# Optimization experiments

Measured on AMD Instinct MI355X. Metric: run time of the kernel, lower is better.

Reference implementation:

```python
import jax, jax.numpy as jnp
import numpy as np

W = 1024          # hpm.W (Fourier window size)
D = 2 * W         # real-ified dimension
BATCH = 2048
P = 8             # number of previous windows
OMEGA = 50        # sparsity level kept by hard threshold
N_ITERS = 10
L = 1.0           # hpm.L (Lipschitz constant, non-learnable)
CLAMP = 150.0


def setup_inputs() -> dict:
    key = jax.random.key(0)
    k1, k2, k3 = jax.random.split(key, 3)
    x = jax.random.normal(k1, (BATCH, D), jnp.float32)
    prev_windows = jax.random.normal(k2, (P, BATCH, D), jnp.float32)
    # learnable dictionary (Fourier-initialized in the original; random orthogonal-ish here)
    W_d = jax.random.normal(k3, (D, D), jnp.float32) / np.float32(np.sqrt(D))
    # S = I - (1/L) W_d^T W_d, exactly as in __init__
    S = jnp.eye(D, dtype=jnp.float32) - (1.0 / L) * (W_d.T @ W_d)
    lambda2 = jnp.array(1.0, jnp.float32)
    return {"x": x, "prev_windows": prev_windows, "W_d": W_d, "S": S, "lambda2": lambda2}


def _hard_thr(v):
    # keep the OMEGA largest-|.| entries along the last axis, zero the rest
    a = jnp.abs(v)
    kth = jax.lax.top_k(a, OMEGA)[0][..., -1:]  # (batch, 1) threshold
    return jnp.where(a >= kth, v, jnp.zeros_like(v))


def reference(x, prev_windows, W_d, S, lambda2):
    # B = (1/L) W_d x         (batch, D); z vectors kept as (batch, D), last dim == the
    # original dim=-2 since trailing singleton dim is squeezed away.
    B = (1.0 / L) * jnp.einsum('ij,bj->bi', W_d, x)
    z = _hard_thr(B)
    z = _hard_thr(B + jnp.einsum('ij,bj->bi', S, z))

    # attention over previous windows
    s_t = jnp.einsum('ji,bj->bi', W_d, z)                       # W_d^T z : (batch, D)
    s_prev = jnp.einsum('ij,pbj->pbi', W_d, prev_windows)       # (P, batch, D)
    # diagonal of (P,batch,batch) matmul == per-(p,b) dot product; compute it directly
    att = jnp.einsum('pbd,bd->pb', s_prev, s_t)                 # (P, batch)
    att = jax.nn.softmax(att, axis=1)
    pw = jnp.clip(prev_windows, -CLAMP, CLAMP)
    z = lambda2 * jnp.sum(pw * att[..., None], axis=0)          # (batch, D)

    # LIHT iterations; only zs[-1] is used downstream, so carry only the last z
    def step(zc, _):
        zn = _hard_thr(B + jnp.einsum('ij,bj->bi', S, zc))
        return zn, None
    z_last, _ = jax.lax.scan(step, z, None, length=N_ITERS)

    # complex power spectrum: sign flip on imag part does not change the norm
    cpx = z_last.reshape(BATCH, 2, W)
    p = cpx[:, 0, :] ** 2 + cpx[:, 1, :] ** 2                   # (batch, W)
    mD = p.sum(0)                                               # (W,)
    mD_norm = (mD - mD.min()) / (mD.max() - mD.min() + 1e-8)
    return mD_norm, z_last
```

## Files before the change

kernel.cpp:

```cpp
#include <hip/hip_runtime.h>


#define DD 2048
#define NB 2048
#define PLANE ((size_t)1 << 22)
#define ZONE 49152

using short8v  = __attribute__((ext_vector_type(8))) short;
using ushort8v = __attribute__((ext_vector_type(8))) unsigned short;
using ushort4v = __attribute__((ext_vector_type(4))) unsigned short;
using float4v  = __attribute__((ext_vector_type(4))) float;

__device__ __forceinline__ unsigned short f2bf(float f) {
  unsigned u = __float_as_uint(f);
  u = u + 0x7fffu + ((u >> 16) & 1u);
  return (unsigned short)(u >> 16);
}
__device__ __forceinline__ float bf2f(unsigned short h) {
  return __uint_as_float((unsigned)h << 16);
}
__device__ __forceinline__ void gload16(const void* g, void* l) {
  __builtin_amdgcn_global_load_lds((const __attribute__((address_space(1))) void*)g,
                                   (__attribute__((address_space(3))) void*)l,
                                   16, 0, 0);
}

template<int R>
__global__ __launch_bounds__(256)
void conv3T(const float* __restrict__ in, unsigned short* __restrict__ p0,
            unsigned short* __restrict__ p1, unsigned short* __restrict__ p2) {
  __shared__ unsigned short lds3[3][4][R][8];
  const int rt = blockIdx.x, c = blockIdx.y, t = threadIdx.x;
  const int cf = (t & 7) * 4;
  const int g = cf >> 3, e0 = cf & 7;
#pragma unroll
  for (int pass = 0; pass < R / 32; ++pass) {
    const int r = pass * 32 + (t >> 3);
    float4 v = *(const float4*)(in + (size_t)(rt * R + r) * DD + c * 32 + cf);
    float vv[4] = {v.x, v.y, v.z, v.w};
    ushort4v o0, o1, o2;
#pragma unroll
    for (int j = 0; j < 4; ++j) {
      unsigned short a0 = f2bf(vv[j]); float r1 = vv[j] - bf2f(a0);
      unsigned short a1 = f2bf(r1);    float r2 = r1 - bf2f(a1);
      unsigned short a2 = f2bf(r2);
      o0[j] = a0; o1[j] = a1; o2[j] = a2;
    }
    *(ushort4v*)&lds3[0][g][r][e0] = o0;
    *(ushort4v*)&lds3[1][g][r][e0] = o1;
    *(ushort4v*)&lds3[2][g][r][e0] = o2;
  }
  __syncthreads();
  const ushort8v* src = (const ushort8v*)lds3;
  const size_t tb = ((size_t)rt * 64 + c) * (R * 32);
#pragma unroll
  for (int w = 0; w < (3 * R) / 64; ++w) {
    const int idx = w * 256 + t;
    const int p = idx / (4 * R), off = idx % (4 * R);
    unsigned short* dst = (p == 0 ? p0 : p == 1 ? p1 : p2) + tb + (size_t)off * 8;
    *(ushort8v*)dst = src[idx];
  }
}

__global__ __launch_bounds__(256)
void tconv3(const float* __restrict__ in, unsigned short* __restrict__ p0,
            unsigned short* __restrict__ p1, unsigned short* __restrict__ p2) {
  __shared__ unsigned short lds3[3][4][64][8];
  const int nt = blockIdx.x, c = blockIdx.y, t = threadIdx.x;
  const int nf = (t & 15) * 4;
#pragma unroll
  for (int pass = 0; pass < 2; ++pass) {
    const int kr = pass * 16 + (t >> 4);
    float4 v = *(const float4*)(in + (size_t)(c * 32 + kr) * DD + nt * 64 + nf);
    float vv[4] = {v.x, v.y, v.z, v.w};
    const int g = kr >> 3, e = kr & 7;
#pragma unroll
    for (int j = 0; j < 4; ++j) {
      unsigned short a0 = f2bf(vv[j]); float r1 = vv[j] - bf2f(a0);
      unsigned short a1 = f2bf(r1);    float r2 = r1 - bf2f(a1);
      unsigned short a2 = f2bf(r2);
      lds3[0][g][nf + j][e] = a0;
      lds3[1][g][nf + j][e] = a1;
      lds3[2][g][nf + j][e] = a2;
    }
  }
  __syncthreads();
  const ushort8v* src = (const ushort8v*)lds3;
  const size_t tb = ((size_t)nt * 64 + c) * 2048;
#pragma unroll
  for (int w = 0; w < 3; ++w) {
    const int idx = w * 256 + t;
    const int p = idx >> 8, off = idx & 255;
    unsigned short* dst = (p == 0 ? p0 : p == 1 ? p1 : p2) + tb + (size_t)off * 8;
    *(ushort8v*)dst = src[idx];
  }
}

template<int ADD>
__global__ __launch_bounds__(512)
void gemm_bf6(const unsigned short* __restrict__ PA,
              const unsigned short* __restrict__ PB,
              const float* __restrict__ Cadd, float* __restrict__ Cout) {
  __shared__ char lds[3 * ZONE];
  const int tid = threadIdx.x, lane = tid & 63, wid = tid >> 6;

  const int lin = (int)blockIdx.x;
  const int xcd = lin & 7, q = lin >> 3;
  const int mt = (xcd >> 1) * 4 + (q >> 3);
  const int nt = (xcd & 1) * 8 + (q & 7);
  const int m0 = mt * 128, n0 = nt * 128;

  auto stage = [&](char* base, int c) {
    if (wid < 4) {
      const size_t at = ((size_t)mt * 64 + c) * 4096;
#pragma unroll
      for (int i = 0; i < 6; ++i) {
        const int slot = wid * 6 + i, p = slot >> 3, j = slot & 7;
        gload16(PA + p * PLANE + at + j * 512 + lane * 8,
                base + p * 8192 + j * 1024 + lane * 16);
      }
    } else {
#pragma unroll
      for (int i = 0; i < 6; ++i) {
        const int b = (wid - 4) * 6 + i, p = b >> 3, r = b & 7;
        const int sub = r >> 2, j = r & 3;
        const size_t bt = ((size_t)(nt * 2 + sub) * 64 + c) * 2048;
        gload16(PB + p * PLANE + bt + j * 512 + lane * 8,
                base + 24576 + p * 8192 + sub * 4096 + j * 1024 + lane * 16);
      }
    }
  };

  float4v acc[4][2] = {};

  const int rsel = (wid >> 2) * 64;
  const int csel = (wid & 3) * 32;
  const int g16  = lane >> 4;
  const int l15  = lane & 15;
  const int aoff = g16 * 2048 + (rsel + l15) * 16;
  const int boff = 24576 + (csel >> 6) * 4096 + g16 * 1024
                 + ((csel & 32) + l15) * 16;

  stage(lds, 0);
  stage(lds + ZONE, 1);

  int zc = 0, zs = 2;
  for (int c = 0; c < 64; ++c) {
    if (c + 2 < 64) stage(lds + zs * ZONE, c + 2);
    if (c + 2 < 64)      asm volatile("s_waitcnt vmcnt(12)" ::: "memory");
    else if (c + 1 < 64) asm volatile("s_waitcnt vmcnt(6)"  ::: "memory");
    else                 asm volatile("s_waitcnt vmcnt(0)"  ::: "memory");
    __builtin_amdgcn_s_barrier();
    __builtin_amdgcn_sched_barrier(0);

    const char* cur = lds + zc * ZONE;
    short8v b0[2], b1[2], b2[2];
#pragma unroll
    for (int ng = 0; ng < 2; ++ng) {
      b0[ng] = *(const short8v*)(cur + boff + 0 * 8192 + ng * 256);
      b1[ng] = *(const short8v*)(cur + boff + 1 * 8192 + ng * 256);
      b2[ng] = *(const short8v*)(cur + boff + 2 * 8192 + ng * 256);
    }
#pragma unroll
    for (int mg = 0; mg < 4; ++mg) {
      const short8v a0 = *(const short8v*)(cur + 0 * 8192 + aoff + mg * 256);
      const short8v a1 = *(const short8v*)(cur + 1 * 8192 + aoff + mg * 256);
      const short8v a2 = *(const short8v*)(cur + 2 * 8192 + aoff + mg * 256);
#pragma unroll
      for (int ng = 0; ng < 2; ++ng) {
        float4v t = acc[mg][ng];
        t = __builtin_amdgcn_mfma_f32_16x16x32_bf16(a0, b0[ng], t, 0, 0, 0);
        t = __builtin_amdgcn_mfma_f32_16x16x32_bf16(a0, b1[ng], t, 0, 0, 0);
        t = __builtin_amdgcn_mfma_f32_16x16x32_bf16(a1, b0[ng], t, 0, 0, 0);
        t = __builtin_amdgcn_mfma_f32_16x16x32_bf16(a1, b1[ng], t, 0, 0, 0);
        t = __builtin_amdgcn_mfma_f32_16x16x32_bf16(a0, b2[ng], t, 0, 0, 0);
        t = __builtin_amdgcn_mfma_f32_16x16x32_bf16(a2, b0[ng], t, 0, 0, 0);
        acc[mg][ng] = t;
      }
    }
    __builtin_amdgcn_sched_barrier(0);
    __builtin_amdgcn_s_barrier();
    zc = (zc == 2) ? 0 : zc + 1;
    zs = (zs == 2) ? 0 : zs + 1;
  }

  const int row0 = m0 + rsel + g16 * 4;
  const int col0 = n0 + csel + l15;
#pragma unroll
  for (int mg = 0; mg < 4; ++mg)
#pragma unroll
    for (int ng = 0; ng < 2; ++ng)
#pragma unroll
      for (int r = 0; r < 4; ++r) {
        const size_t o = (size_t)(row0 + mg * 16 + r) * DD + col0 + ng * 16;
        float v = acc[mg][ng][r];
        if (ADD) v += Cadd[o];
        Cout[o] = v;
      }
}

template<int HASBASE>
__global__ __launch_bounds__(64)
void spapply_sl(const float* __restrict__ M, const float* __restrict__ baseB,
                float* __restrict__ outF, const unsigned* __restrict__ sidx,
                const float* __restrict__ sval, const int* __restrict__ scnt) {
  const int b = blockIdx.y, lane = threadIdx.x;
  const int col = blockIdx.x * 256 + lane * 4;
  const int nc = scnt[b];
  const unsigned* ip = sidx + b * 64;
  const float* vp = sval + b * 64;
  const size_t ro = (size_t)b * DD + col;
  float4 a;
  if (HASBASE) a = *(const float4*)&baseB[ro];
  else         a = make_float4(0.f, 0.f, 0.f, 0.f);
  for (int t = 0; t < nc; ++t) {
    const unsigned j = ip[t];
    const float v = vp[t];
    float4 m = *(const float4*)&M[(size_t)j * DD + col];
    a.x = fmaf(v, m.x, a.x); a.y = fmaf(v, m.y, a.y);
    a.z = fmaf(v, m.z, a.z); a.w = fmaf(v, m.w, a.w);
  }
  *(float4*)&outF[ro] = a;
}

__global__ __launch_bounds__(64)
void topk_kernel(const float* __restrict__ src, unsigned* __restrict__ sidx,
                 float* __restrict__ sval, int* __restrict__ scnt,
                 float* __restrict__ dense, float* __restrict__ mD,
                 int finalMode) {
  const int b = blockIdx.x;
  const int lane = threadIdx.x;
  const float* row = src + (size_t)b * DD;
  float v[32]; unsigned ab[32];
#pragma unroll
  for (int e4 = 0; e4 < 8; ++e4) {
    float4 t = *(const float4*)&row[e4*256 + lane*4];
    v[e4*4+0]=t.x; v[e4*4+1]=t.y; v[e4*4+2]=t.z; v[e4*4+3]=t.w;
  }
#pragma unroll
  for (int e = 0; e < 32; ++e) ab[e] = __float_as_uint(v[e]) & 0x7fffffffu;

  unsigned mxb = 0;
#pragma unroll
  for (int e = 0; e < 32; ++e) mxb = ab[e] > mxb ? ab[e] : mxb;
  for (int off = 32; off; off >>= 1) {
    unsigned o = (unsigned)__shfl_down((int)mxb, off);
    mxb = o > mxb ? o : mxb;
  }
  mxb = (unsigned)__shfl((int)mxb, 0);
  const int emax = (int)(mxb >> 23);

  int eStar = 0, cntAbove = 0;
  {
    int prevc = 0;
    for (int e = emax; e >= 0; --e) {
      unsigned T = ((unsigned)e) << 23;
      int c = 0;
#pragma unroll
      for (int k = 0; k < 32; ++k) c += (ab[k] >= T) ? 1 : 0;
      for (int off = 32; off; off >>= 1) c += __shfl_down(c, off);
      c = __shfl(c, 0);
      if (c >= 50) { eStar = e; cntAbove = prevc; break; }
      prevc = c;
    }
  }
  unsigned kth = ((unsigned)eStar) << 23;
  int kneed = 50 - cntAbove;

  __shared__ int hist[256];
  __shared__ int sh_sel, sh_kneed;
  for (int p = 0; p < 3; ++p) {
    const unsigned mask = (p==0) ? 0x7F800000u : (p==1) ? 0x7FFF8000u : 0x7FFFFF80u;
    const int sh = (p==0) ? 15 : (p==1) ? 7 : 0;
    for (int t = lane; t < 256; t += 64) hist[t] = 0;
    __syncthreads();
#pragma unroll
    for (int e = 0; e < 32; ++e)
      if ((ab[e] & mask) == kth) atomicAdd(&hist[(ab[e] >> sh) & 0xFF], 1);
    __syncthreads();
    int h0 = hist[lane*4+0], h1 = hist[lane*4+1], h2 = hist[lane*4+2], h3 = hist[lane*4+3];
    int s = h0 + h1 + h2 + h3;
    int x = s;
    for (int off = 1; off < 64; off <<= 1) {
      int y = __shfl_down(x, off);
      if (lane + off < 64) x += y;
    }
    int excl = x - s;
    int c3 = excl + h3, c2 = c3 + h2, c1 = c2 + h1, c0 = c1 + h0;
    if (c0 >= kneed && c1   < kneed) { sh_sel = lane*4+0; sh_kneed = kneed - c1;  }
    if (c1 >= kneed && c2   < kneed) { sh_sel = lane*4+1; sh_kneed = kneed - c2;  }
    if (c2 >= kneed && c3   < kneed) { sh_sel = lane*4+2; sh_kneed = kneed - c3;  }
    if (c3 >= kneed && excl < kneed) { sh_sel = lane*4+3; sh_kneed = kneed - excl;}
    __syncthreads();
    kth |= ((unsigned)sh_sel) << sh;
    kneed = sh_kneed;
    __syncthreads();
  }

  int base = 0;
#pragma unroll
  for (int e4 = 0; e4 < 8; ++e4) {
    float o[4];
#pragma unroll
    for (int qq = 0; qq < 4; ++qq) {
      const int e = e4*4 + qq;
      const bool sel = ab[e] >= kth;
      unsigned long long msk = __ballot(sel);
      int pre = __popcll(msk & ((1ull << lane) - 1ull));
      const unsigned gi = (unsigned)(e4*256 + lane*4 + qq);
      if (sel) {
        int slot = base + pre;
        if (slot < 64) { sidx[b*64+slot] = gi; sval[b*64+slot] = v[e]; }
        if (finalMode) atomicAdd(&mD[gi & 1023u], v[e]*v[e]);
      }
      base += __popcll(msk);
      o[qq] = sel ? v[e] : 0.f;
    }
    if (finalMode) {
      float4 t = {o[0],o[1],o[2],o[3]};
      *(float4*)&dense[(size_t)b*DD + e4*256 + lane*4] = t;
    }
  }
  if (lane == 0) scnt[b] = base < 64 ? base : 64;
}

__global__ __launch_bounds__(256)
void attdot_kernel(const float* __restrict__ prev, const float* __restrict__ U,
                   float* __restrict__ att) {
  const int b = blockIdx.x, p = blockIdx.y, tid = threadIdx.x;
  const float* pr = prev + ((size_t)p*NB + b) * DD;
  const float* u  = U + (size_t)b * DD;
  float s = 0.f;
#pragma unroll
  for (int h = 0; h < 2; ++h) {
    int i = (tid + h*256) * 4;
    float4 a = *(const float4*)&pr[i];
    float4 c = *(const float4*)&u[i];
    s += a.x*c.x + a.y*c.y + a.z*c.z + a.w*c.w;
  }
  for (int off = 32; off; off >>= 1) s += __shfl_down(s, off);
  __shared__ float ps[4];
  if ((tid & 63) == 0) ps[tid >> 6] = s;
  __syncthreads();
  if (tid == 0) att[(size_t)p*NB + b] = ps[0]+ps[1]+ps[2]+ps[3];
}

__global__ __launch_bounds__(256)
void softmax_kernel(const float* __restrict__ att, float* __restrict__ attw) {
  const int p = blockIdx.x, tid = threadIdx.x;
  const float* a = att + (size_t)p*NB;
  float loc[8]; float mx = -3.4e38f;
#pragma unroll
  for (int h = 0; h < 8; ++h) { loc[h] = a[tid + h*256]; mx = fmaxf(mx, loc[h]); }
  for (int off = 32; off; off >>= 1) mx = fmaxf(mx, __shfl_down(mx, off));
  __shared__ float ps[4]; __shared__ float sh_m, sh_s;
  if ((tid & 63) == 0) ps[tid >> 6] = mx;
  __syncthreads();
  if (tid == 0) sh_m = fmaxf(fmaxf(ps[0],ps[1]), fmaxf(ps[2],ps[3]));
  __syncthreads();
  const float m = sh_m;
  float sum = 0.f;
#pragma unroll
  for (int h = 0; h < 8; ++h) sum += expf(loc[h] - m);
  for (int off = 32; off; off >>= 1) sum += __shfl_down(sum, off);
  __syncthreads();
  if ((tid & 63) == 0) ps[tid >> 6] = sum;
  __syncthreads();
  if (tid == 0) sh_s = ps[0]+ps[1]+ps[2]+ps[3];
  __syncthreads();
  const float inv = 1.0f / sh_s;
#pragma unroll
  for (int h = 0; h < 8; ++h) attw[(size_t)p*NB + tid + h*256] = expf(loc[h] - m) * inv;
}

__global__ __launch_bounds__(256)
void zatt_kernel(const float* __restrict__ prev, const float* __restrict__ attw,
                 const float* __restrict__ lam, float* __restrict__ Z) {
  const int b = blockIdx.x, tid = threadIdx.x;
  __shared__ float w[8];
  if (tid < 8) w[tid] = attw[(size_t)tid*NB + b];
  __syncthreads();
  const float l2 = lam[0];
#pragma unroll
  for (int h = 0; h < 2; ++h) {
    int i = (tid + h*256) * 4;
    float4 acc = {0.f,0.f,0.f,0.f};
#pragma unroll
    for (int p = 0; p < 8; ++p) {
      float4 pv = *(const float4*)&prev[((size_t)p*NB + b)*DD + i];
      float wp = w[p];
      acc.x += wp * fminf(fmaxf(pv.x, -150.f), 150.f);
      acc.y += wp * fminf(fmaxf(pv.y, -150.f), 150.f);
      acc.z += wp * fminf(fmaxf(pv.z, -150.f), 150.f);
      acc.w += wp * fminf(fmaxf(pv.w, -150.f), 150.f);
    }
    acc.x *= l2; acc.y *= l2; acc.z *= l2; acc.w *= l2;
    *(float4*)&Z[(size_t)b*DD + i] = acc;
  }
}

__global__ __launch_bounds__(256)
void norm_kernel(float* __restrict__ mD) {
  const int tid = threadIdx.x;
  float v[4]; float mn = 3.4e38f, mx = -3.4e38f;
#pragma unroll
  for (int h = 0; h < 4; ++h) {
    v[h] = mD[tid + h*256];
    mn = fminf(mn, v[h]); mx = fmaxf(mx, v[h]);
  }
  for (int off = 32; off; off >>= 1) {
    mn = fminf(mn, __shfl_down(mn, off));
    mx = fmaxf(mx, __shfl_down(mx, off));
  }
  __shared__ float pmn[4], pmx[4]; __shared__ float smn, smx;
  if ((tid & 63) == 0) { pmn[tid>>6] = mn; pmx[tid>>6] = mx; }
  __syncthreads();
  if (tid == 0) {
    smn = fminf(fminf(pmn[0],pmn[1]), fminf(pmn[2],pmn[3]));
    smx = fmaxf(fmaxf(pmx[0],pmx[1]), fmaxf(pmx[2],pmx[3]));
  }
  __syncthreads();
  const float d = smx - smn + 1e-8f;
#pragma unroll
  for (int h = 0; h < 4; ++h) mD[tid + h*256] = (v[h] - smn) / d;
}

extern "C" void kernel_launch(void* const* d_in, const int* in_sizes, int n_in,
                              void* d_out, int out_size, void* d_ws, size_t ws_size,
                              hipStream_t stream) {
  const float* x    = (const float*)d_in[0];
  const float* prev = (const float*)d_in[1];
  const float* Wd   = (const float*)d_in[2];
  const float* S    = (const float*)d_in[3];
  const float* lam  = (const float*)d_in[4];

  float* out   = (float*)d_out;
  float* mD    = out;
  float* zlast = out + 1024;

  float* B  = (float*)d_ws;
  float* C  = B  + (1u << 22);
  float* X1 = C  + (1u << 22);
  unsigned* sidx = (unsigned*)(X1 + (1u << 22));
  float*    sval = (float*)(sidx + 2048*64);
  int*      scnt = (int*)(sval + 2048*64);
  float*    att  = (float*)(scnt + 2048);
  float*    attw = att + 8*2048;
  unsigned short* PA = (unsigned short*)(attw + 8*2048);
  unsigned short* PB = PA + 3 * PLANE;
  float* U = zlast;

  const dim3 gSp(8, NB);
  const dim3 gA(16, 64);
  const dim3 gB(32, 64);

  conv3T<128><<<gA, 256, 0, stream>>>(x,  PA, PA + PLANE, PA + 2*PLANE);
  conv3T<64> <<<gB, 256, 0, stream>>>(Wd, PB, PB + PLANE, PB + 2*PLANE);
  gemm_bf6<0><<<256, 512, 0, stream>>>(PA, PB, nullptr, B);
  topk_kernel<<<NB, 64, 0, stream>>>(B, sidx, sval, scnt, nullptr, nullptr, 0);
  spapply_sl<1><<<gSp, 64, 0, stream>>>(S, B, C, sidx, sval, scnt);
  topk_kernel<<<NB, 64, 0, stream>>>(C, sidx, sval, scnt, nullptr, nullptr, 0);
  spapply_sl<0><<<gSp, 64, 0, stream>>>(Wd, nullptr, X1, sidx, sval, scnt);
  conv3T<128><<<gA, 256, 0, stream>>>(X1, PA, PA + PLANE, PA + 2*PLANE);
  tconv3<<<gB, 256, 0, stream>>>(Wd, PB, PB + PLANE, PB + 2*PLANE);
  gemm_bf6<0><<<256, 512, 0, stream>>>(PA, PB, nullptr, U);
  attdot_kernel<<<dim3(NB, 8), 256, 0, stream>>>(prev, U, att);
  softmax_kernel<<<8, 256, 0, stream>>>(att, attw);
  zatt_kernel<<<NB, 256, 0, stream>>>(prev, attw, lam, X1);
  conv3T<128><<<gA, 256, 0, stream>>>(X1, PA, PA + PLANE, PA + 2*PLANE);
  conv3T<64> <<<gB, 256, 0, stream>>>(S,  PB, PB + PLANE, PB + 2*PLANE);
  gemm_bf6<1><<<256, 512, 0, stream>>>(PA, PB, B, C);
  topk_kernel<<<NB, 64, 0, stream>>>(C, sidx, sval, scnt, nullptr, nullptr, 0);
  for (int it = 1; it < 10; ++it) {
    spapply_sl<1><<<gSp, 64, 0, stream>>>(S, B, C, sidx, sval, scnt);
    const int fin = (it == 9);
    if (fin) hipMemsetAsync(mD, 0, 1024 * sizeof(float), stream);
    topk_kernel<<<NB, 64, 0, stream>>>(C, sidx, sval, scnt,
                                       fin ? zlast : nullptr,
                                       fin ? mD : nullptr, fin);
  }
  norm_kernel<<<1, 256, 0, stream>>>(mD);
}
```

Baseline: 1.218 ms.

## Use 4-wave GEMM tiles with single barrier and pipeline sparse row gathers

The bf16x3 GEMM now runs 256 threads per block. Each wave computes a 64x64 sub-tile, up from 64x32, so every A fragment feeds twice as many MFMAs. The next-stage prefetch is issued after the barrier, which drops the second per-iteration barrier, and the vmcnt waits are adjusted to match. The sparse-apply kernel now packs four rows per 256-thread block, stages the indices and values in LDS, and software-pipelines eight gathered float4 loads to raise memory-level parallelism. The trade-off is higher register pressure from the 4x4 accumulators and fewer waves per CU for the GEMM, plus the risk that one barrier per iteration is not enough to guard the triple-buffer reuse.

```diff
diff --git a/kernel.cpp b/kernel.cpp
--- a/kernel.cpp
+++ b/kernel.cpp
@@ -97,7 +97,7 @@
 }
 
 template<int ADD>
-__global__ __launch_bounds__(512)
+__global__ __launch_bounds__(256)
 void gemm_bf6(const unsigned short* __restrict__ PA,
               const unsigned short* __restrict__ PB,
               const float* __restrict__ Cadd, float* __restrict__ Cout) {
@@ -111,18 +111,18 @@
   const int m0 = mt * 128, n0 = nt * 128;
 
   auto stage = [&](char* base, int c) {
-    if (wid < 4) {
+    if (wid < 2) {
       const size_t at = ((size_t)mt * 64 + c) * 4096;
 #pragma unroll
-      for (int i = 0; i < 6; ++i) {
-        const int slot = wid * 6 + i, p = slot >> 3, j = slot & 7;
+      for (int i = 0; i < 12; ++i) {
+        const int slot = wid * 12 + i, p = slot >> 3, j = slot & 7;
         gload16(PA + p * PLANE + at + j * 512 + lane * 8,
                 base + p * 8192 + j * 1024 + lane * 16);
       }
     } else {
 #pragma unroll
-      for (int i = 0; i < 6; ++i) {
-        const int b = (wid - 4) * 6 + i, p = b >> 3, r = b & 7;
+      for (int i = 0; i < 12; ++i) {
+        const int bq = (wid - 2) * 12 + i, p = bq >> 3, r = bq & 7;
         const int sub = r >> 2, j = r & 3;
         const size_t bt = ((size_t)(nt * 2 + sub) * 64 + c) * 2048;
         gload16(PB + p * PLANE + bt + j * 512 + lane * 8,
@@ -131,32 +131,31 @@
     }
   };
 
-  float4v acc[4][2] = {};
-
-  const int rsel = (wid >> 2) * 64;
-  const int csel = (wid & 3) * 32;
+  float4v acc[4][4] = {};
+
+  const int rsel = (wid >> 1) * 64;
+  const int csel = (wid & 1) * 64;
   const int g16  = lane >> 4;
   const int l15  = lane & 15;
   const int aoff = g16 * 2048 + (rsel + l15) * 16;
-  const int boff = 24576 + (csel >> 6) * 4096 + g16 * 1024
-                 + ((csel & 32) + l15) * 16;
+  const int boff = 24576 + (csel >> 6) * 4096 + g16 * 1024 + l15 * 16;
 
   stage(lds, 0);
   stage(lds + ZONE, 1);
 
   int zc = 0, zs = 2;
   for (int c = 0; c < 64; ++c) {
-    if (c + 2 < 64) stage(lds + zs * ZONE, c + 2);
-    if (c + 2 < 64)      asm volatile("s_waitcnt vmcnt(12)" ::: "memory");
-    else if (c + 1 < 64) asm volatile("s_waitcnt vmcnt(6)"  ::: "memory");
-    else                 asm volatile("s_waitcnt vmcnt(0)"  ::: "memory");
+    if (c < 63) asm volatile("s_waitcnt vmcnt(12)" ::: "memory");
+    else        asm volatile("s_waitcnt vmcnt(0)"  ::: "memory");
     __builtin_amdgcn_s_barrier();
     __builtin_amdgcn_sched_barrier(0);
 
+    if (c + 2 < 64) stage(lds + zs * ZONE, c + 2);
+
     const char* cur = lds + zc * ZONE;
-    short8v b0[2], b1[2], b2[2];
-#pragma unroll
-    for (int ng = 0; ng < 2; ++ng) {
+    short8v b0[4], b1[4], b2[4];
+#pragma unroll
+    for (int ng = 0; ng < 4; ++ng) {
       b0[ng] = *(const short8v*)(cur + boff + 0 * 8192 + ng * 256);
       b1[ng] = *(const short8v*)(cur + boff + 1 * 8192 + ng * 256);
       b2[ng] = *(const short8v*)(cur + boff + 2 * 8192 + ng * 256);
@@ -167,7 +166,7 @@
       const short8v a1 = *(const short8v*)(cur + 1 * 8192 + aoff + mg * 256);
       const short8v a2 = *(const short8v*)(cur + 2 * 8192 + aoff + mg * 256);
 #pragma unroll
-      for (int ng = 0; ng < 2; ++ng) {
+      for (int ng = 0; ng < 4; ++ng) {
         float4v t = acc[mg][ng];
         t = __builtin_amdgcn_mfma_f32_16x16x32_bf16(a0, b0[ng], t, 0, 0, 0);
         t = __builtin_amdgcn_mfma_f32_16x16x32_bf16(a0, b1[ng], t, 0, 0, 0);
@@ -178,8 +177,6 @@
         acc[mg][ng] = t;
       }
     }
-    __builtin_amdgcn_sched_barrier(0);
-    __builtin_amdgcn_s_barrier();
     zc = (zc == 2) ? 0 : zc + 1;
     zs = (zs == 2) ? 0 : zs + 1;
   }
@@ -189,7 +186,7 @@
 #pragma unroll
   for (int mg = 0; mg < 4; ++mg)
 #pragma unroll
-    for (int ng = 0; ng < 2; ++ng)
+    for (int ng = 0; ng < 4; ++ng)
 #pragma unroll
       for (int r = 0; r < 4; ++r) {
         const size_t o = (size_t)(row0 + mg * 16 + r) * DD + col0 + ng * 16;
@@ -200,25 +197,54 @@
 }
 
 template<int HASBASE>
-__global__ __launch_bounds__(64)
+__global__ __launch_bounds__(256)
 void spapply_sl(const float* __restrict__ M, const float* __restrict__ baseB,
                 float* __restrict__ outF, const unsigned* __restrict__ sidx,
                 const float* __restrict__ sval, const int* __restrict__ scnt) {
-  const int b = blockIdx.y, lane = threadIdx.x;
+  const int lane = threadIdx.x & 63, w = threadIdx.x >> 6;
+  const int b = blockIdx.y * 4 + w;
   const int col = blockIdx.x * 256 + lane * 4;
+  __shared__ unsigned sj[4][64];
+  __shared__ float    sv[4][64];
+  sj[w][lane] = sidx[b * 64 + lane];
+  sv[w][lane] = sval[b * 64 + lane];
   const int nc = scnt[b];
-  const unsigned* ip = sidx + b * 64;
-  const float* vp = sval + b * 64;
+  __syncthreads();
+
   const size_t ro = (size_t)b * DD + col;
   float4 a;
   if (HASBASE) a = *(const float4*)&baseB[ro];
   else         a = make_float4(0.f, 0.f, 0.f, 0.f);
-  for (int t = 0; t < nc; ++t) {
-    const unsigned j = ip[t];
-    const float v = vp[t];
-    float4 m = *(const float4*)&M[(size_t)j * DD + col];
+
+  const float* Mc = M + col;
+  auto ld = [&](int t) -> float4 {
+    return *(const float4*)(Mc + (size_t)sj[w][t] * DD);
+  };
+  auto fma4 = [&](int t, const float4& m) {
+    const float v = sv[w][t];
     a.x = fmaf(v, m.x, a.x); a.y = fmaf(v, m.y, a.y);
     a.z = fmaf(v, m.z, a.z); a.w = fmaf(v, m.w, a.w);
+  };
+
+  float4 m[8];
+  int t = 0;
+  if (nc >= 8) {
+#pragma unroll
+    for (int i = 0; i < 8; ++i) m[i] = ld(i);
+    for (; t + 16 <= nc; t += 8) {
+#pragma unroll
+      for (int i = 0; i < 8; ++i) {
+        fma4(t + i, m[i]);
+        m[i] = ld(t + 8 + i);
+      }
+    }
+#pragma unroll
+    for (int i = 0; i < 8; ++i) fma4(t + i, m[i]);
+    t += 8;
+  }
+  for (; t < nc; ++t) {
+    float4 mm = ld(t);
+    fma4(t, mm);
   }
   *(float4*)&outF[ro] = a;
 }
@@ -450,29 +476,29 @@
   unsigned short* PB = PA + 3 * PLANE;
   float* U = zlast;
 
-  const dim3 gSp(8, NB);
+  const dim3 gSp(8, NB / 4);
   const dim3 gA(16, 64);
   const dim3 gB(32, 64);
 
   conv3T<128><<<gA, 256, 0, stream>>>(x,  PA, PA + PLANE, PA + 2*PLANE);
   conv3T<64> <<<gB, 256, 0, stream>>>(Wd, PB, PB + PLANE, PB + 2*PLANE);
-  gemm_bf6<0><<<256, 512, 0, stream>>>(PA, PB, nullptr, B);
+  gemm_bf6<0><<<256, 256, 0, stream>>>(PA, PB, nullptr, B);
   topk_kernel<<<NB, 64, 0, stream>>>(B, sidx, sval, scnt, nullptr, nullptr, 0);
-  spapply_sl<1><<<gSp, 64, 0, stream>>>(S, B, C, sidx, sval, scnt);
+  spapply_sl<1><<<gSp, 256, 0, stream>>>(S, B, C, sidx, sval, scnt);
   topk_kernel<<<NB, 64, 0, stream>>>(C, sidx, sval, scnt, nullptr, nullptr, 0);
-  spapply_sl<0><<<gSp, 64, 0, stream>>>(Wd, nullptr, X1, sidx, sval, scnt);
+  spapply_sl<0><<<gSp, 256, 0, stream>>>(Wd, nullptr, X1, sidx, sval, scnt);
   conv3T<128><<<gA, 256, 0, stream>>>(X1, PA, PA + PLANE, PA + 2*PLANE);
   tconv3<<<gB, 256, 0, stream>>>(Wd, PB, PB + PLANE, PB + 2*PLANE);
-  gemm_bf6<0><<<256, 512, 0, stream>>>(PA, PB, nullptr, U);
+  gemm_bf6<0><<<256, 256, 0, stream>>>(PA, PB, nullptr, U);
   attdot_kernel<<<dim3(NB, 8), 256, 0, stream>>>(prev, U, att);
   softmax_kernel<<<8, 256, 0, stream>>>(att, attw);
   zatt_kernel<<<NB, 256, 0, stream>>>(prev, attw, lam, X1);
   conv3T<128><<<gA, 256, 0, stream>>>(X1, PA, PA + PLANE, PA + 2*PLANE);
   conv3T<64> <<<gB, 256, 0, stream>>>(S,  PB, PB + PLANE, PB + 2*PLANE);
-  gemm_bf6<1><<<256, 512, 0, stream>>>(PA, PB, B, C);
+  gemm_bf6<1><<<256, 256, 0, stream>>>(PA, PB, B, C);
   topk_kernel<<<NB, 64, 0, stream>>>(C, sidx, sval, scnt, nullptr, nullptr, 0);
   for (int it = 1; it < 10; ++it) {
-    spapply_sl<1><<<gSp, 64, 0, stream>>>(S, B, C, sidx, sval, scnt);
+    spapply_sl<1><<<gSp, 256, 0, stream>>>(S, B, C, sidx, sval, scnt);
     const int fin = (it == 9);
     if (fin) hipMemsetAsync(mD, 0, 1024 * sizeof(float), stream);
     topk_kernel<<<NB, 64, 0, stream>>>(C, sidx, sval, scnt,
```

After: 1.098 ms. -9.9%, faster.
